# Kernel tuning notes

Measured on AMD Instinct MI355X. Metric: run time of the kernel, lower is better.

The kernel has to match this reference:

```python
import jax, jax.numpy as jnp
import numpy as np

H = 256
B, S = 8, 2048
WIN = 16


def setup_inputs() -> dict:
    key = jax.random.key(0)
    k1, k2, k3, k4, k5 = jax.random.split(key, 5)
    bound = 1.0 / np.sqrt(H)  # torch nn.RNN init range
    x = jax.random.normal(k1, (B, S, H), dtype=jnp.float32)
    W_ih = jax.random.uniform(k2, (H, H), jnp.float32, -bound, bound)
    W_hh = jax.random.uniform(k3, (H, H), jnp.float32, -bound, bound)
    b_ih = jax.random.uniform(k4, (H,), jnp.float32, -bound, bound)
    b_hh = jax.random.uniform(k5, (H,), jnp.float32, -bound, bound)
    return {"x": x, "W_ih": W_ih, "W_hh": W_hh, "b_ih": b_ih, "b_hh": b_hh, "window": WIN}


def reference(x, W_ih, W_hh, b_ih, b_hh, window):
    # Original: get_K builds [B, S, window, H] overlapping windows (left-padded
    # with window-1 zeros), runs an RNN over each length-`window` sequence with
    # h0 = 0, and keeps the last hidden state -> [B, S, H].
    # Equivalent streaming form: at step k of the window, every position t
    # consumes xpad[:, t + k]; so slice a shifted view of the padded input and
    # update all B*S hidden states at once (never materializing the windows).
    b, s, h = x.shape
    xpad = jnp.pad(x, ((0, 0), (window - 1, 0), (0, 0)))  # [B, S+W-1, H]

    def step(hid, k):
        xk = jax.lax.dynamic_slice(xpad, (0, k, 0), (b, s, h))  # [B, S, H]
        hid = jnp.tanh(xk @ W_ih.T + b_ih + hid @ W_hh.T + b_hh)
        return hid, None

    h0 = jnp.zeros((b, s, h), dtype=x.dtype)
    h_last, _ = jax.lax.scan(step, h0, jnp.arange(window))
    return h_last  # [B, S, H]
```

## Files before the change

### kernel.cpp

```cpp
#include <hip/hip_runtime.h>

#define HDIM 256
#define SEQ 2048

typedef _Float16 half8_t __attribute__((ext_vector_type(8)));
typedef _Float16 half4_t __attribute__((ext_vector_type(4)));
typedef float floatx16 __attribute__((ext_vector_type(16)));

#define U_PITCH 512
#define H_PITCH 512
#define U_ROWS 79
#define HA0_OFF (U_ROWS * U_PITCH)
#define LDS_BYTES (HA0_OFF + 4 * 16384)

static __device__ __forceinline__ float exp2f_fast(float x) {
  float r; asm("v_exp_f32 %0, %1" : "=v"(r) : "v"(x)); return r;
}
static __device__ __forceinline__ float rcpf_fast(float x) {
  float r; asm("v_rcp_f32 %0, %1" : "=v"(r) : "v"(x)); return r;
}
static __device__ __forceinline__ float tanhf_fast(float x) {
  float e = exp2f_fast(x * 2.8853900817779268f);
  return 1.0f - 2.0f * rcpf_fast(e + 1.0f);
}
static __device__ __forceinline__ unsigned pkh(float a, float b) {
  return __builtin_bit_cast(unsigned, __builtin_amdgcn_cvt_pkrtz(a, b));
}

__global__ __launch_bounds__(512, 1) void winrnn_kernel(
    const float* __restrict__ x, const float* __restrict__ W_ih,
    const float* __restrict__ W_hh, const float* __restrict__ b_ih,
    const float* __restrict__ b_hh, float* __restrict__ out) {
  extern __shared__ char smem[];
  const int tid = threadIdx.x;
  const int w = tid >> 6;
  const int lane = tid & 63;
  const int l31 = lane & 31;
  const int hi = lane >> 5;

  const int wg = blockIdx.x;
  const int batch = wg >> 5;
  const int t0 = (wg & 31) * 64;
  const float* xb = x + (size_t)batch * SEQ * HDIM;

  const int t = w & 1;
  const int jbase = (w >> 1) * 64;
  const int tb = t * 32;
  const int hswz = l31 << 4;

  char* const hbuf = smem + HA0_OFF + t * 32768;

  {
    char* xl = smem + HA0_OFF;
#pragma unroll
    for (int it = 0; it < 12; ++it) {
      int idx = tid + it * 512;
      int row = idx >> 6;
      int c4 = idx & 63;
      int xi = t0 - 15 + row;
      float4 v = make_float4(0.f, 0.f, 0.f, 0.f);
      if (row < U_ROWS && xi >= 0)
        v = *reinterpret_cast<const float4*>(xb + (size_t)xi * HDIM + c4 * 4);
      uint2 u;
      u.x = pkh(v.x, v.y);
      u.y = pkh(v.z, v.w);
      *reinterpret_cast<uint2*>(xl + row * H_PITCH + ((c4 * 8) ^ ((row & 31) << 4))) = u;
    }
  }

  half8_t Wf[2][16];
#pragma unroll
  for (int jt = 0; jt < 2; ++jt)
#pragma unroll
    for (int kt = 0; kt < 16; ++kt) {
      const float* wp = W_ih + (size_t)(jbase + jt * 32 + l31) * HDIM + kt * 16 + hi * 8;
      float4 a = *reinterpret_cast<const float4*>(wp);
      float4 b = *reinterpret_cast<const float4*>(wp + 4);
      uint4 uu;
      uu.x = pkh(a.x, a.y); uu.y = pkh(a.z, a.w);
      uu.z = pkh(b.x, b.y); uu.w = pkh(b.z, b.w);
      Wf[jt][kt] = __builtin_bit_cast(half8_t, uu);
    }

  float4 biasf[2][4];
#pragma unroll
  for (int jt = 0; jt < 2; ++jt)
#pragma unroll
    for (int g = 0; g < 4; ++g) {
      int j0 = jbase + jt * 32 + g * 8 + hi * 4;
      float4 bi = *reinterpret_cast<const float4*>(b_ih + j0);
      float4 bh = *reinterpret_cast<const float4*>(b_hh + j0);
      biasf[jt][g] = make_float4(bi.x + bh.x, bi.y + bh.y, bi.z + bh.z, bi.w + bh.w);
    }

  __syncthreads();

  {
    const char* xl = smem + HA0_OFF;
    char* Ul = smem;
    for (int s = t; s < 3; s += 2) {
      int prow = s * 32 + l31;
      floatx16 acc0, acc1;
#pragma unroll
      for (int g = 0; g < 4; ++g) {
        acc0[4*g+0] = biasf[0][g].x; acc0[4*g+1] = biasf[0][g].y;
        acc0[4*g+2] = biasf[0][g].z; acc0[4*g+3] = biasf[0][g].w;
        acc1[4*g+0] = biasf[1][g].x; acc1[4*g+1] = biasf[1][g].y;
        acc1[4*g+2] = biasf[1][g].z; acc1[4*g+3] = biasf[1][g].w;
      }
#pragma unroll
      for (int kt = 0; kt < 16; ++kt) {
        half8_t xB = *reinterpret_cast<const half8_t*>(
            xl + prow * H_PITCH + ((kt * 32 + hi * 16) ^ ((prow & 31) << 4)));
        acc0 = __builtin_amdgcn_mfma_f32_32x32x16_f16(Wf[0][kt], xB, acc0, 0, 0, 0);
        acc1 = __builtin_amdgcn_mfma_f32_32x32x16_f16(Wf[1][kt], xB, acc1, 0, 0, 0);
      }
      if (prow < U_ROWS) {
        int uswz = (prow & 31) << 4;
#pragma unroll
        for (int jt = 0; jt < 2; ++jt)
#pragma unroll
          for (int g = 0; g < 4; ++g) {
            const floatx16& ac = jt ? acc1 : acc0;
            uint2 st;
            st.x = pkh(ac[4*g+0], ac[4*g+1]);
            st.y = pkh(ac[4*g+2], ac[4*g+3]);
            int j0 = jbase + jt * 32 + g * 8 + hi * 4;
            *reinterpret_cast<uint2*>(Ul + prow * U_PITCH + ((j0 * 2) ^ uswz)) = st;
          }
      }
    }
  }

#pragma unroll
  for (int jt = 0; jt < 2; ++jt)
#pragma unroll
    for (int kt = 0; kt < 16; ++kt) {
      const float* wp = W_hh + (size_t)(jbase + jt * 32 + l31) * HDIM + kt * 16 + hi * 8;
      float4 a = *reinterpret_cast<const float4*>(wp);
      float4 b = *reinterpret_cast<const float4*>(wp + 4);
      uint4 uu;
      uu.x = pkh(a.x, a.y); uu.y = pkh(a.z, a.w);
      uu.z = pkh(b.x, b.y); uu.w = pkh(b.z, b.w);
      Wf[jt][kt] = __builtin_bit_cast(half8_t, uu);
    }

  __syncthreads();

  const char* Ul = smem;
  floatx16 acc0, acc1;
  for (int k = 0; k < 16; ++k) {
    const int urow = tb + l31 + k;
    const int uswz = (urow & 31) << 4;
#pragma unroll
    for (int g = 0; g < 4; ++g) {
      int j00 = (jbase + g * 8 + hi * 4) * 2;
      half4_t u0 = __builtin_bit_cast(half4_t, *reinterpret_cast<const uint2*>(
          Ul + urow * U_PITCH + (j00 ^ uswz)));
      half4_t u1 = __builtin_bit_cast(half4_t, *reinterpret_cast<const uint2*>(
          Ul + urow * U_PITCH + ((j00 + 64) ^ uswz)));
      acc0[4*g+0] = (float)u0[0]; acc0[4*g+1] = (float)u0[1];
      acc0[4*g+2] = (float)u0[2]; acc0[4*g+3] = (float)u0[3];
      acc1[4*g+0] = (float)u1[0]; acc1[4*g+1] = (float)u1[1];
      acc1[4*g+2] = (float)u1[2]; acc1[4*g+3] = (float)u1[3];
    }
    if (k > 0) {
      const char* hr = hbuf + ((k & 1) ? 0 : 16384);
#pragma unroll
      for (int kt = 0; kt < 16; ++kt) {
        half8_t hB = *reinterpret_cast<const half8_t*>(
            hr + l31 * H_PITCH + ((kt * 32 + hi * 16) ^ hswz));
        acc0 = __builtin_amdgcn_mfma_f32_32x32x16_f16(Wf[0][kt], hB, acc0, 0, 0, 0);
        acc1 = __builtin_amdgcn_mfma_f32_32x32x16_f16(Wf[1][kt], hB, acc1, 0, 0, 0);
      }
    }
    if (k < 15) {
      char* hw = hbuf + ((k & 1) ? 16384 : 0);
#pragma unroll
      for (int jt = 0; jt < 2; ++jt) {
        const floatx16& ac = jt ? acc1 : acc0;
#pragma unroll
        for (int g = 0; g < 4; ++g) {
          float ta = tanhf_fast(ac[4*g+0]);
          float tb2 = tanhf_fast(ac[4*g+1]);
          float tc = tanhf_fast(ac[4*g+2]);
          float td = tanhf_fast(ac[4*g+3]);
          uint2 u; u.x = pkh(ta, tb2); u.y = pkh(tc, td);
          int jb = (jbase + jt * 32 + g * 8 + hi * 4) * 2;
          *reinterpret_cast<uint2*>(hw + l31 * H_PITCH + (jb ^ hswz)) = u;
        }
      }
      __syncthreads();
    }
  }

  __syncthreads();
  {
    char* ol = smem + HA0_OFF;
    const int orow = tb + l31;
    const int oswz = (orow & 31) << 4;
#pragma unroll
    for (int jt = 0; jt < 2; ++jt) {
      const floatx16& ac = jt ? acc1 : acc0;
#pragma unroll
      for (int g = 0; g < 4; ++g) {
        float4 st;
        st.x = tanhf_fast(ac[4*g+0]); st.y = tanhf_fast(ac[4*g+1]);
        st.z = tanhf_fast(ac[4*g+2]); st.w = tanhf_fast(ac[4*g+3]);
        int jb4 = (jbase + jt * 32 + g * 8 + hi * 4) * 4;
        *reinterpret_cast<float4*>(ol + orow * 1024 + (jb4 ^ oswz)) = st;
      }
    }
  }
  __syncthreads();
  {
    const char* ol = smem + HA0_OFF;
    float* ob = out + ((size_t)batch * SEQ + t0) * HDIM;
#pragma unroll
    for (int it = 0; it < 8; ++it) {
      int idx = tid + it * 512;
      int row = idx >> 6;
      int c = idx & 63;
      float4 v = *reinterpret_cast<const float4*>(
          ol + row * 1024 + ((c * 16) ^ ((row & 31) << 4)));
      *reinterpret_cast<float4*>(ob + (size_t)row * HDIM + c * 4) = v;
    }
  }
}

extern "C" void kernel_launch(void* const* d_in, const int* in_sizes, int n_in,
                              void* d_out, int out_size, void* d_ws, size_t ws_size,
                              hipStream_t stream) {
  const float* x    = (const float*)d_in[0];
  const float* W_ih = (const float*)d_in[1];
  const float* W_hh = (const float*)d_in[2];
  const float* b_ih = (const float*)d_in[3];
  const float* b_hh = (const float*)d_in[4];
  float* out = (float*)d_out;
  static_assert(LDS_BYTES <= 160 * 1024, "LDS budget");
  hipFuncSetAttribute(reinterpret_cast<const void*>(winrnn_kernel),
                      hipFuncAttributeMaxDynamicSharedMemorySize, LDS_BYTES);
  winrnn_kernel<<<dim3(256), dim3(512), LDS_BYTES, stream>>>(x, W_ih, W_hh, b_ih, b_hh, out);
}
```

Baseline: 73.93 us.

## Split recurrent MFMA chains, keep U in fp32, prefetch next-step U rows

Splits each 16-deep dependent MFMA accumulation chain into two independent 8-deep chains, summed before tanh, to shorten per-step MFMA latency. Stores the input projection U in fp32 instead of fp16, doubling its LDS pitch. The next step's U row is loaded into registers before the tanh/store phase so LDS latency overlaps other work. In exchange it uses more accumulator registers and more LDS.

```diff
diff --git a/kernel.cpp b/kernel.cpp
--- a/kernel.cpp
+++ b/kernel.cpp
@@ -4,14 +4,13 @@
 #define SEQ 2048
 
 typedef _Float16 half8_t __attribute__((ext_vector_type(8)));
-typedef _Float16 half4_t __attribute__((ext_vector_type(4)));
 typedef float floatx16 __attribute__((ext_vector_type(16)));
 
-#define U_PITCH 512
+#define U_PITCH 1024
 #define H_PITCH 512
 #define U_ROWS 79
 #define HA0_OFF (U_ROWS * U_PITCH)
-#define LDS_BYTES (HA0_OFF + 4 * 16384)
+#define LDS_BYTES (HA0_OFF + 65536)
 
 static __device__ __forceinline__ float exp2f_fast(float x) {
   float r; asm("v_exp_f32 %0, %1" : "=v"(r) : "v"(x)); return r;
@@ -47,7 +46,6 @@
   const int jbase = (w >> 1) * 64;
   const int tb = t * 32;
   const int hswz = l31 << 4;
-
   char* const hbuf = smem + HA0_OFF + t * 32768;
 
   {
@@ -122,11 +120,10 @@
 #pragma unroll
           for (int g = 0; g < 4; ++g) {
             const floatx16& ac = jt ? acc1 : acc0;
-            uint2 st;
-            st.x = pkh(ac[4*g+0], ac[4*g+1]);
-            st.y = pkh(ac[4*g+2], ac[4*g+3]);
             int j0 = jbase + jt * 32 + g * 8 + hi * 4;
-            *reinterpret_cast<uint2*>(Ul + prow * U_PITCH + ((j0 * 2) ^ uswz)) = st;
+            float4 st;
+            st.x = ac[4*g+0]; st.y = ac[4*g+1]; st.z = ac[4*g+2]; st.w = ac[4*g+3];
+            *reinterpret_cast<float4*>(Ul + prow * U_PITCH + ((j0 * 4) ^ uswz)) = st;
           }
       }
     }
@@ -148,51 +145,76 @@
   __syncthreads();
 
   const char* Ul = smem;
-  floatx16 acc0, acc1;
+  floatx16 acc0, acc0b, acc1, acc1b;
+  float4 uq0[4], uq1[4];
+  {
+    const int urow = tb + l31;
+    const int uswz = (urow & 31) << 4;
+#pragma unroll
+    for (int g = 0; g < 4; ++g) {
+      int j00 = (jbase + g * 8 + hi * 4) * 4;
+      uq0[g] = *reinterpret_cast<const float4*>(Ul + urow * U_PITCH + (j00 ^ uswz));
+      uq1[g] = *reinterpret_cast<const float4*>(Ul + urow * U_PITCH + ((j00 + 128) ^ uswz));
+    }
+  }
+
   for (int k = 0; k < 16; ++k) {
-    const int urow = tb + l31 + k;
-    const int uswz = (urow & 31) << 4;
 #pragma unroll
     for (int g = 0; g < 4; ++g) {
-      int j00 = (jbase + g * 8 + hi * 4) * 2;
-      half4_t u0 = __builtin_bit_cast(half4_t, *reinterpret_cast<const uint2*>(
-          Ul + urow * U_PITCH + (j00 ^ uswz)));
-      half4_t u1 = __builtin_bit_cast(half4_t, *reinterpret_cast<const uint2*>(
-          Ul + urow * U_PITCH + ((j00 + 64) ^ uswz)));
-      acc0[4*g+0] = (float)u0[0]; acc0[4*g+1] = (float)u0[1];
-      acc0[4*g+2] = (float)u0[2]; acc0[4*g+3] = (float)u0[3];
-      acc1[4*g+0] = (float)u1[0]; acc1[4*g+1] = (float)u1[1];
-      acc1[4*g+2] = (float)u1[2]; acc1[4*g+3] = (float)u1[3];
+      acc0[4*g+0] = uq0[g].x; acc0[4*g+1] = uq0[g].y;
+      acc0[4*g+2] = uq0[g].z; acc0[4*g+3] = uq0[g].w;
+      acc1[4*g+0] = uq1[g].x; acc1[4*g+1] = uq1[g].y;
+      acc1[4*g+2] = uq1[g].z; acc1[4*g+3] = uq1[g].w;
+      acc0b[4*g+0] = 0.f; acc0b[4*g+1] = 0.f; acc0b[4*g+2] = 0.f; acc0b[4*g+3] = 0.f;
+      acc1b[4*g+0] = 0.f; acc1b[4*g+1] = 0.f; acc1b[4*g+2] = 0.f; acc1b[4*g+3] = 0.f;
     }
     if (k > 0) {
       const char* hr = hbuf + ((k & 1) ? 0 : 16384);
 #pragma unroll
-      for (int kt = 0; kt < 16; ++kt) {
-        half8_t hB = *reinterpret_cast<const half8_t*>(
-            hr + l31 * H_PITCH + ((kt * 32 + hi * 16) ^ hswz));
-        acc0 = __builtin_amdgcn_mfma_f32_32x32x16_f16(Wf[0][kt], hB, acc0, 0, 0, 0);
-        acc1 = __builtin_amdgcn_mfma_f32_32x32x16_f16(Wf[1][kt], hB, acc1, 0, 0, 0);
+      for (int kt = 0; kt < 8; ++kt) {
+        int off0 = (kt * 32 + hi * 16) ^ hswz;
+        int off1 = ((kt + 8) * 32 + hi * 16) ^ hswz;
+        half8_t h0 = *reinterpret_cast<const half8_t*>(hr + l31 * H_PITCH + off0);
+        half8_t h1 = *reinterpret_cast<const half8_t*>(hr + l31 * H_PITCH + off1);
+        acc0  = __builtin_amdgcn_mfma_f32_32x32x16_f16(Wf[0][kt],     h0, acc0,  0, 0, 0);
+        acc0b = __builtin_amdgcn_mfma_f32_32x32x16_f16(Wf[0][kt + 8], h1, acc0b, 0, 0, 0);
+        acc1  = __builtin_amdgcn_mfma_f32_32x32x16_f16(Wf[1][kt],     h0, acc1,  0, 0, 0);
+        acc1b = __builtin_amdgcn_mfma_f32_32x32x16_f16(Wf[1][kt + 8], h1, acc1b, 0, 0, 0);
       }
     }
     if (k < 15) {
+      {
+        const int urow = tb + l31 + k + 1;
+        const int uswz = (urow & 31) << 4;
+#pragma unroll
+        for (int g = 0; g < 4; ++g) {
+          int j00 = (jbase + g * 8 + hi * 4) * 4;
+          uq0[g] = *reinterpret_cast<const float4*>(Ul + urow * U_PITCH + (j00 ^ uswz));
+          uq1[g] = *reinterpret_cast<const float4*>(Ul + urow * U_PITCH + ((j00 + 128) ^ uswz));
+        }
+      }
       char* hw = hbuf + ((k & 1) ? 16384 : 0);
 #pragma unroll
-      for (int jt = 0; jt < 2; ++jt) {
-        const floatx16& ac = jt ? acc1 : acc0;
-#pragma unroll
-        for (int g = 0; g < 4; ++g) {
-          float ta = tanhf_fast(ac[4*g+0]);
-          float tb2 = tanhf_fast(ac[4*g+1]);
-          float tc = tanhf_fast(ac[4*g+2]);
-          float td = tanhf_fast(ac[4*g+3]);
-          uint2 u; u.x = pkh(ta, tb2); u.y = pkh(tc, td);
-          int jb = (jbase + jt * 32 + g * 8 + hi * 4) * 2;
-          *reinterpret_cast<uint2*>(hw + l31 * H_PITCH + (jb ^ hswz)) = u;
-        }
+      for (int g = 0; g < 4; ++g) {
+        float a0 = tanhf_fast(acc0[4*g+0] + acc0b[4*g+0]);
+        float a1 = tanhf_fast(acc0[4*g+1] + acc0b[4*g+1]);
+        float a2 = tanhf_fast(acc0[4*g+2] + acc0b[4*g+2]);
+        float a3 = tanhf_fast(acc0[4*g+3] + acc0b[4*g+3]);
+        float b0 = tanhf_fast(acc1[4*g+0] + acc1b[4*g+0]);
+        float b1 = tanhf_fast(acc1[4*g+1] + acc1b[4*g+1]);
+        float b2 = tanhf_fast(acc1[4*g+2] + acc1b[4*g+2]);
+        float b3 = tanhf_fast(acc1[4*g+3] + acc1b[4*g+3]);
+        int jb = (jbase + g * 8 + hi * 4) * 2;
+        uint2 u0; u0.x = pkh(a0, a1); u0.y = pkh(a2, a3);
+        uint2 u1; u1.x = pkh(b0, b1); u1.y = pkh(b2, b3);
+        *reinterpret_cast<uint2*>(hw + l31 * H_PITCH + (jb ^ hswz)) = u0;
+        *reinterpret_cast<uint2*>(hw + l31 * H_PITCH + ((jb + 64) ^ hswz)) = u1;
       }
       __syncthreads();
     }
   }
+  acc0 += acc0b;
+  acc1 += acc1b;
 
   __syncthreads();
   {
```

Measured after the change: 77.68 us. 5.1% more time.
